# Optimization experiments

Hardware: AMD Instinct MI355X
Metric: run time of the kernel (lower is better)

The kernel has to match this reference:

```python
import jax, jax.numpy as jnp
import numpy as np

SIGNAL_SIZE = 33554432  # 2**25
N_ELEMENTS = 25         # log2(SIGNAL_SIZE)


def fft_shift(a, shift):
    # Faithful port of the torch fft_shift (note: 'shift' variable is reused
    # in the original; the phase ramp overwrites it after shift_samples).
    shift = 1.0 - shift
    n_samples = a.shape[-1]
    shift_samples = shift * n_samples * 0.5
    spec = jnp.fft.rfft(a, norm='ortho')
    n_coeffs = spec.shape[-1]
    phase = jnp.arange(n_coeffs) * (2j * np.pi / n_coeffs)  # complex64 ramp
    spec = spec * jnp.exp(phase * shift_samples)
    return jnp.fft.irfft(spec, n=n_samples, norm='ortho')


def setup_inputs() -> dict:
    key = jax.random.key(0)
    elements = jax.random.uniform(key, (N_ELEMENTS,), minval=-1.0, maxval=1.0,
                                  dtype=jnp.float32)
    return {"elements": elements}


def reference(elements):
    # dirac impulse of size 2 at position 0
    signal = jnp.zeros(2, dtype=jnp.float32).at[0].set(1.0)
    for i in range(N_ELEMENTS):  # fixed trip count; sizes double each step
        if i > 0:
            new_signal = jnp.zeros(signal.shape[-1] * 2, dtype=signal.dtype)
            signal = new_signal.at[::2].set(signal)
        shift_factor = 1.0 / (2 ** i)
        signal = fft_shift(signal, elements[i] * shift_factor)
    return signal  # shape [SIGNAL_SIZE]
```

## Files before the change

### kernel.cpp

```cpp
#include <hip/hip_runtime.h>


constexpr float PI_F    = 3.14159265358979323846f;
constexpr float TWOPI_F = 6.28318530717958647692f;
constexpr unsigned M24 = 1u << 24;

__device__ __forceinline__ void phase_sincos(float th, float* sn, float* cs) {
    double d = (double)th * 0.15915494309189533577;
    d -= rint(d);
    float ang = (float)(d * 6.2831853071795864769);
    __sincosf(ang, sn, cs);
}

__device__ __forceinline__ float2 cmul(float2 a, float2 f) {
    return make_float2(a.x * f.x - a.y * f.y, a.x * f.y + a.y * f.x);
}

__device__ __forceinline__ int xcd_swizzle(int b, int nblocks) {
    int chunk = nblocks >> 3;
    return (b & 7) * chunk + (b >> 3);
}

__global__ __launch_bounds__(256) void build_q(const float* __restrict__ el,
                                               float2* __restrict__ Q) {
    __shared__ float c_s[18], s_s[18], T_s[18];
    int tid = threadIdx.x;
    if (tid < 18) {
        float e = el[tid];
        float shift1 = e * (1.0f / (float)(1u << tid));
        float sh2 = 1.0f - shift1;
        float s = sh2 * (float)(1u << tid);
        float c = (float)(6.2831853071795864769 / (double)((1u << tid) + 1u));
        c_s[tid] = c;
        s_s[tid] = s;
        float p  = (float)(1u << tid) * c;
        float th = p * s;
        float sn, cs; phase_sincos(th, &sn, &cs);
        T_s[tid] = cs;
    }
    __syncthreads();

    unsigned r = blockIdx.x * 256u + (unsigned)tid;
    if (r == 0u) { Q[0] = make_float2(1.0f, 0.0f); return; }

    unsigned t = (unsigned)__builtin_ctz(r);
    float Pr = T_s[t], Pi = 0.0f;

#pragma unroll
    for (int i = 1; i <= 17; ++i) {
        unsigned hi = 1u << i;
        int sd = (int)((r + hi) & (2u * hi - 1u)) - (int)hi;
        int K  = (i <= (int)t) ? 0 : (sd < 0 ? -sd : sd);
        float sgn = (sd < 0) ? -1.0f : 1.0f;
        float p  = (float)K * c_s[i];
        float th = p * s_s[i];
        float sn, cs; phase_sincos(th, &sn, &cs);
        float ssn = sgn * sn;
        float nr = Pr * cs - Pi * ssn;
        float ni = Pr * ssn + Pi * cs;
        Pr = nr; Pi = ni;
    }
    Q[r] = make_float2(Pr, Pi);
}

__device__ __forceinline__ float2 chain_factor(int i, unsigned k,
                                               const float* __restrict__ c_s,
                                               const float* __restrict__ s_s) {
    unsigned hi = 1u << i;
    int sd = (int)((k + hi) & (2u * hi - 1u)) - (int)hi;
    int K  = (sd < 0) ? -sd : sd;
    float sgn = (sd < 0) ? -1.0f : 1.0f;
    float p  = (float)K * c_s[i];
    float th = p * s_s[i];
    float sn, cs; phase_sincos(th, &sn, &cs);
    return make_float2(cs, sgn * sn);
}

struct WPair { float2 wk, wmk; };

__device__ __forceinline__ WPair chain_tail(unsigned k, float Pr, float Pi,
                                            const float* __restrict__ c_s,
                                            const float* __restrict__ s_s) {
    const float sc = 1.0f / 33554432.0f;
    unsigned mk = M24 - k;
    float thk = ((float)k  * c_s[24]) * s_s[24];
    float thm = ((float)mk * c_s[24]) * s_s[24];
    float snk, csk, snm, csm;
    phase_sincos(thk, &snk, &csk);
    phase_sincos(thm, &snm, &csm);

    float Skr = Pr * csk - Pi * snk;
    float Ski = Pr * snk + Pi * csk;
    float Smr = Pr * csm + Pi * snm;
    float Smi = Pr * snm - Pi * csm;

    float Ar = Skr + Smr, Ai = Ski - Smi;
    float Br = Skr - Smr, Bi = Ski + Smi;
    float ang = (float)k * (TWOPI_F / 33554432.0f);
    float ts, tc; __sincosf(ang, &ts, &tc);
    float Cr = tc * Br - ts * Bi;
    float Ci = ts * Br + tc * Bi;

    WPair w;
    w.wk  = make_float2((Ar - Ci) * sc, (Ai + Cr) * sc);
    w.wmk = make_float2((Ar + Ci) * sc, (Cr - Ai) * sc);
    return w;
}

__device__ __forceinline__ WPair chain_W(unsigned k,
                                         const float* __restrict__ c_s,
                                         const float* __restrict__ s_s,
                                         const float* __restrict__ T_s,
                                         const float2* __restrict__ Q) {
    unsigned t = (unsigned)__builtin_ctz(k);
    unsigned r = k & 0x3FFFFu;
    float Pr, Pi;
    if (r != 0u) {
        float2 q = Q[r];
        Pr = q.x; Pi = q.y;
    } else {
        Pr = T_s[t]; Pi = 0.0f;
    }
#pragma unroll
    for (int i = 18; i <= 23; ++i) {
        unsigned hi = 1u << i;
        int sd = (int)((k + hi) & (2u * hi - 1u)) - (int)hi;
        int K  = (i <= (int)t) ? 0 : (sd < 0 ? -sd : sd);
        float sgn = (sd < 0) ? -1.0f : 1.0f;
        float p  = (float)K * c_s[i];
        float th = p * s_s[i];
        float sn, cs; phase_sincos(th, &sn, &cs);
        float ssn = sgn * sn;
        float nr = Pr * cs - Pi * ssn;
        float ni = Pr * ssn + Pi * cs;
        Pr = nr; Pi = ni;
    }
    return chain_tail(k, Pr, Pi, c_s, s_s);
}

__device__ __forceinline__ void bf4(float2* __restrict__ row, int e0, int d,
                                    float2 tw, float2 tw2) {
    float2 x0 = row[e0], x1 = row[e0 + d], x2 = row[e0 + 2*d], x3 = row[e0 + 3*d];
    float2 a0 = make_float2(x0.x + x2.x, x0.y + x2.y);
    float2 d0 = make_float2(x0.x - x2.x, x0.y - x2.y);
    float2 a1 = make_float2(x1.x + x3.x, x1.y + x3.y);
    float2 d1 = make_float2(x1.x - x3.x, x1.y - x3.y);
    float2 a2 = make_float2(d0.x * tw.x - d0.y * tw.y,  d0.x * tw.y + d0.y * tw.x);
    float2 a3 = make_float2(-d1.x * tw.y - d1.y * tw.x, d1.x * tw.x - d1.y * tw.y);
    row[e0]       = make_float2(a0.x + a1.x, a0.y + a1.y);
    float2 u1 = make_float2(a0.x - a1.x, a0.y - a1.y);
    row[e0 + d]   = make_float2(u1.x * tw2.x - u1.y * tw2.y, u1.x * tw2.y + u1.y * tw2.x);
    row[e0 + 2*d] = make_float2(a2.x + a3.x, a2.y + a3.y);
    float2 u3 = make_float2(a2.x - a3.x, a2.y - a3.y);
    row[e0 + 3*d] = make_float2(u3.x * tw2.x - u3.y * tw2.y, u3.x * tw2.y + u3.y * tw2.x);
}

__device__ __forceinline__ void fft256x16_inv(float2 (*lds)[257], int tid) {
    {
        int j2 = tid & 63;
        float s, c; __sincosf((PI_F / 128.0f) * (float)j2, &s, &c);
        float2 tw  = make_float2(c, s);
        float2 tw2 = make_float2(c * c - s * s, 2.0f * c * s);
        __syncthreads();
#pragma unroll
        for (int v = 0; v < 4; ++v) {
            int row = (tid >> 6) + 4 * v;
            bf4(lds[row], j2, 64, tw, tw2);
        }
    }
    {
        int rowb = tid & 15;
        int j2   = tid >> 4;
        float s, c; __sincosf((PI_F / 32.0f) * (float)j2, &s, &c);
        float2 tw  = make_float2(c, s);
        float2 tw2 = make_float2(c * c - s * s, 2.0f * c * s);
        __syncthreads();
#pragma unroll
        for (int v = 0; v < 4; ++v) {
            bf4(lds[rowb], 64 * v + j2, 16, tw, tw2);
        }
    }
    {
        int rowb = tid & 15;
        int j2   = tid >> 6;
        int bbl  = (tid >> 4) & 3;
        float s, c; __sincosf((PI_F / 8.0f) * (float)j2, &s, &c);
        float2 tw  = make_float2(c, s);
        float2 tw2 = make_float2(c * c - s * s, 2.0f * c * s);
        __syncthreads();
#pragma unroll
        for (int v = 0; v < 4; ++v) {
            int bb = bbl + 4 * v;
            bf4(lds[rowb], 16 * bb + j2, 4, tw, tw2);
        }
    }
    {
        int rowb = tid & 15;
        int bbl  = tid >> 4;
        __syncthreads();
#pragma unroll
        for (int v = 0; v < 4; ++v) {
            int e0 = 4 * (bbl + 16 * v);
            float2* row = lds[rowb];
            float2 x0 = row[e0], x1 = row[e0 + 1], x2 = row[e0 + 2], x3 = row[e0 + 3];
            float2 a0 = make_float2(x0.x + x2.x, x0.y + x2.y);
            float2 d0 = make_float2(x0.x - x2.x, x0.y - x2.y);
            float2 a1 = make_float2(x1.x + x3.x, x1.y + x3.y);
            float2 d1 = make_float2(x1.x - x3.x, x1.y - x3.y);
            row[e0]     = make_float2(a0.x + a1.x, a0.y + a1.y);
            row[e0 + 1] = make_float2(a0.x - a1.x, a0.y - a1.y);
            row[e0 + 2] = make_float2(d0.x - d1.y, d0.y + d1.x);
            row[e0 + 3] = make_float2(d0.x + d1.y, d0.y - d1.x);
        }
    }
    __syncthreads();
}

__device__ __forceinline__ int c_of_row(int b, int r) {
    if (b == 0) {
        if (r < 8)  return r;
        if (r == 8) return 32768;
        return 65536 - (r - 8);
    }
    return (r < 8) ? (8 * b + r) : (65536 - 8 * b - (r - 8));
}

__global__ __launch_bounds__(256, 4) void fused_build_fft_a(const float* __restrict__ el,
                                                            const float2* __restrict__ Q,
                                                            float2* __restrict__ out) {
    __shared__ float2 lds[16][257];
    __shared__ float c_s[25], s_s[25], T_s[24];
    int tid = threadIdx.x;
    if (tid < 25) {
        float e = el[tid];
        float shift1 = e * (1.0f / (float)(1u << tid));
        float sh2 = 1.0f - shift1;
        float s = sh2 * (float)(1u << tid);
        float c = (float)(6.2831853071795864769 / (double)((1u << tid) + 1u));
        c_s[tid] = c;
        s_s[tid] = s;
        if (tid < 24) {
            float p  = (float)(1u << tid) * c;
            float th = p * s;
            float sn, cs; phase_sincos(th, &sn, &cs);
            T_s[tid] = cs;
        }
    }
    __syncthreads();

    int b   = xcd_swizzle(blockIdx.x, 4096);
    int r   = tid & 15;
    int k30 = tid >> 4;
    int c   = c_of_row(b, r);
    int rm  = (b == 0 && (r == 0 || r == 8)) ? r : (r ^ 8);

    if (b == 0 && r == 0) {
#pragma unroll 1
        for (int u = 0; u < 8; ++u) {
            int k3 = k30 + 16 * u;
            if (k3 == 0) {
                float p  = 16777216.0f * c_s[24];
                float th = p * s_s[24];
                float sn, cs; phase_sincos(th, &sn, &cs);
                const float sc = 1.0f / 33554432.0f;
                lds[0][0] = make_float2((1.0f + cs) * sc, (1.0f - cs) * sc);
                WPair w = chain_W(8388608u, c_s, s_s, T_s, Q);
                lds[0][128] = w.wk;
            } else {
                unsigned j = (unsigned)k3 << 16;
                WPair w = chain_W(j, c_s, s_s, T_s, Q);
                lds[0][k3] = w.wk;
                lds[0][256 - k3] = w.wmk;
            }
        }
    } else {
        unsigned kbase = (unsigned)c + ((unsigned)k30 << 16);
        unsigned rres  = kbase & 0x3FFFFu;
        float2 P1 = Q[rres];
        P1 = cmul(P1, chain_factor(18, kbase, c_s, s_s));
        P1 = cmul(P1, chain_factor(19, kbase, c_s, s_s));
        float2 P2[2], P3[4];
#pragma unroll
        for (int j = 0; j < 2; ++j)
            P2[j] = cmul(P1, chain_factor(20, kbase + ((unsigned)j << 20), c_s, s_s));
#pragma unroll
        for (int j = 0; j < 4; ++j)
            P3[j] = cmul(P2[j & 1], chain_factor(21, kbase + ((unsigned)j << 20), c_s, s_s));

#pragma unroll 1
        for (int u = 0; u < 8; ++u) {
            int k3 = k30 + 16 * u;
            unsigned k = kbase + ((unsigned)u << 20);
            float2 P = cmul(P3[u & 3], chain_factor(22, k, c_s, s_s));
            P = cmul(P, chain_factor(23, k, c_s, s_s));
            WPair w = chain_tail(k, P.x, P.y, c_s, s_s);
            lds[r][k3] = w.wk;
            lds[rm][255 - k3] = w.wmk;
        }
    }

    fft256x16_inv(lds, tid);

#pragma unroll
    for (int u = 0; u < 16; ++u) {
        int e = tid + 256 * u;
        int row = e & 15, p = e >> 4;
        int t3 = (int)(__brev((unsigned)p) >> 24);
        int cr = c_of_row(b, row);
        out[cr + (t3 << 16)] = lds[row][p];
    }
}

__global__ __launch_bounds__(256, 4) void fft_stage_b(const float2* __restrict__ in,
                                                      float2* __restrict__ out) {
    __shared__ float2 lds[16][257];
    int tid = threadIdx.x;
    int wg  = xcd_swizzle(blockIdx.x, 4096);
    int k1b = (wg & 15) * 16;
    int t3  = wg >> 4;
    const float tsc = TWOPI_F / 65536.0f;
    {
        int row = tid & 15;
        int k20 = tid >> 4;
        const float2* src = in + (k1b + row + (k20 << 8) + (t3 << 16));
        float2 vbuf[16];
#pragma unroll
        for (int u = 0; u < 16; ++u) vbuf[u] = src[u << 12];
        float sb, cb; __sincosf(tsc * (float)(t3 * k20), &sb, &cb);
        float ss, cs; __sincosf(tsc * (float)(t3 * 16), &ss, &cs);
        float2 w = make_float2(cb, sb);
#pragma unroll
        for (int u = 0; u < 16; ++u) {
            int k2 = k20 + 16 * u;
            float2 v = vbuf[u];
            lds[row][k2] = make_float2(v.x * w.x - v.y * w.y, v.x * w.y + v.y * w.x);
            float nx = w.x * cs - w.y * ss;
            float ny = w.x * ss + w.y * cs;
            w = make_float2(nx, ny);
        }
    }
    fft256x16_inv(lds, tid);
#pragma unroll
    for (int u = 0; u < 16; ++u) {
        int e = tid + 256 * u;
        int row = e & 15, p = e >> 4;
        int t2 = (int)(__brev((unsigned)p) >> 24);
        out[k1b + row + (t2 << 8) + (t3 << 16)] = lds[row][p];
    }
}

__global__ __launch_bounds__(256, 4) void fft_stage_c(const float2* __restrict__ in,
                                                      float2* __restrict__ out) {
    __shared__ float2 lds[16][257];
    int tid = threadIdx.x;
    int wg  = xcd_swizzle(blockIdx.x, 4096);
    int t3b = (wg & 15) * 16;
    int t2  = wg >> 4;
    const float tsc = TWOPI_F / 16777216.0f;
    {
        int k1 = tid;
        const float2* src = in + (k1 + (t2 << 8) + (t3b << 16));
        float2 vbuf[16];
#pragma unroll
        for (int u = 0; u < 16; ++u) vbuf[u] = src[u << 16];
        int base = (t3b + (t2 << 8)) * k1;
        float sb, cb; __sincosf(tsc * (float)base, &sb, &cb);
        float ss, cs; __sincosf(tsc * (float)k1, &ss, &cs);
        float2 w = make_float2(cb, sb);
#pragma unroll
        for (int u = 0; u < 16; ++u) {
            float2 v = vbuf[u];
            lds[u][k1] = make_float2(v.x * w.x - v.y * w.y, v.x * w.y + v.y * w.x);
            float nx = w.x * cs - w.y * ss;
            float ny = w.x * ss + w.y * cs;
            w = make_float2(nx, ny);
        }
    }
    fft256x16_inv(lds, tid);
#pragma unroll
    for (int u = 0; u < 16; ++u) {
        int e = tid + 256 * u;
        int r = e & 15, p = e >> 4;
        int t1 = (int)(__brev((unsigned)p) >> 24);
        out[(t3b + r) + (t2 << 8) + (t1 << 16)] = lds[r][p];
    }
}

extern "C" void kernel_launch(void* const* d_in, const int* in_sizes, int n_in,
                              void* d_out, int out_size, void* d_ws, size_t ws_size,
                              hipStream_t stream) {
    const float* el = (const float*)d_in[0];
    float2* Gd = (float2*)d_out;
    float2* Q  = (float2*)d_ws;

    hipLaunchKernelGGL(build_q,           dim3(1024), dim3(256), 0, stream, el, Q);
    hipLaunchKernelGGL(fused_build_fft_a, dim3(4096), dim3(256), 0, stream, el, Q, Gd);
    hipLaunchKernelGGL(fft_stage_b,       dim3(4096), dim3(256), 0, stream, Gd, (float2*)d_ws);
    hipLaunchKernelGGL(fft_stage_c,       dim3(4096), dim3(256), 0, stream, (float2*)d_ws, Gd);
}
```

Baseline: 278.4 us.

## Replace radix-4 LDS FFT passes with register-resident radix-16 two-pass FFT

Replaces the four-pass radix-4 256-point FFT, which round-trips through shared memory each pass, with a 16x16 decomposition. Each thread holds 16 values in registers, applies a radix-16 butterfly, twiddles, transposes once through LDS, then does a second radix-16 pass. The final bit-reversed LDS readback is dropped and results are written straight to global memory. Stage B also keeps its loaded data in registers for the first pass. Launch bounds drop from 4 to 3 blocks per CU to make room for the larger register footprint. This cuts LDS traffic and barriers at the cost of higher register pressure and less regular store coalescing.

```diff
diff --git a/kernel.cpp b/kernel.cpp
--- a/kernel.cpp
+++ b/kernel.cpp
@@ -1,7 +1,6 @@
 #include <hip/hip_runtime.h>
 
 
-constexpr float PI_F    = 3.14159265358979323846f;
 constexpr float TWOPI_F = 6.28318530717958647692f;
 constexpr unsigned M24 = 1u << 24;
 
@@ -15,10 +14,65 @@
 __device__ __forceinline__ float2 cmul(float2 a, float2 f) {
     return make_float2(a.x * f.x - a.y * f.y, a.x * f.y + a.y * f.x);
 }
+__device__ __forceinline__ float2 caddf(float2 a, float2 b) { return make_float2(a.x + b.x, a.y + b.y); }
+__device__ __forceinline__ float2 csubf(float2 a, float2 b) { return make_float2(a.x - b.x, a.y - b.y); }
+__device__ __forceinline__ float2 cmulw(float2 a, float c, float s) {
+    return make_float2(a.x * c - a.y * s, a.x * s + a.y * c);
+}
 
 __device__ __forceinline__ int xcd_swizzle(int b, int nblocks) {
     int chunk = nblocks >> 3;
     return (b & 7) * chunk + (b >> 3);
+}
+
+__device__ __forceinline__ void fft16_inv(float2* v) {
+    const float C1 = 0.92387953251128675613f;
+    const float S1 = 0.38268343236508977173f;
+    const float R2 = 0.70710678118654752440f;
+    float2 h[16];
+#pragma unroll
+    for (int b = 0; b < 4; ++b) {
+        float2 s02 = caddf(v[b], v[b + 8]);
+        float2 d02 = csubf(v[b], v[b + 8]);
+        float2 s13 = caddf(v[b + 4], v[b + 12]);
+        float2 d13 = csubf(v[b + 4], v[b + 12]);
+        float2 id13 = make_float2(-d13.y, d13.x);
+        h[4 * b + 0] = caddf(s02, s13);
+        h[4 * b + 1] = caddf(d02, id13);
+        h[4 * b + 2] = csubf(s02, s13);
+        h[4 * b + 3] = csubf(d02, id13);
+    }
+    h[5]  = cmulw(h[5],  C1,  S1);
+    h[6]  = make_float2(R2 * (h[6].x - h[6].y),  R2 * (h[6].x + h[6].y));
+    h[7]  = cmulw(h[7],  S1,  C1);
+    h[9]  = make_float2(R2 * (h[9].x - h[9].y),  R2 * (h[9].x + h[9].y));
+    h[10] = make_float2(-h[10].y, h[10].x);
+    h[11] = cmulw(h[11], -R2, R2);
+    h[13] = cmulw(h[13], S1,  C1);
+    h[14] = cmulw(h[14], -R2, R2);
+    h[15] = cmulw(h[15], -C1, -S1);
+#pragma unroll
+    for (int K1 = 0; K1 < 4; ++K1) {
+        float2 a = h[K1], bb = h[4 + K1], cc = h[8 + K1], dd = h[12 + K1];
+        float2 sac = caddf(a, cc), dac = csubf(a, cc);
+        float2 sbd = caddf(bb, dd), dbd = csubf(bb, dd);
+        float2 idbd = make_float2(-dbd.y, dbd.x);
+        v[K1]      = caddf(sac, sbd);
+        v[K1 + 4]  = caddf(dac, idbd);
+        v[K1 + 8]  = csubf(sac, sbd);
+        v[K1 + 12] = csubf(dac, idbd);
+    }
+}
+
+__device__ __forceinline__ void ztwiddle(float2* v, int q) {
+    float ss, cc;
+    __sincosf((TWOPI_F / 256.0f) * (float)q, &ss, &cc);
+    float2 w = make_float2(1.0f, 0.0f), stp = make_float2(cc, ss);
+#pragma unroll
+    for (int K1 = 0; K1 < 16; ++K1) {
+        v[K1] = cmul(v[K1], w);
+        w = cmul(w, stp);
+    }
 }
 
 __global__ __launch_bounds__(256) void build_q(const float* __restrict__ el,
@@ -138,84 +192,6 @@
     return chain_tail(k, Pr, Pi, c_s, s_s);
 }
 
-__device__ __forceinline__ void bf4(float2* __restrict__ row, int e0, int d,
-                                    float2 tw, float2 tw2) {
-    float2 x0 = row[e0], x1 = row[e0 + d], x2 = row[e0 + 2*d], x3 = row[e0 + 3*d];
-    float2 a0 = make_float2(x0.x + x2.x, x0.y + x2.y);
-    float2 d0 = make_float2(x0.x - x2.x, x0.y - x2.y);
-    float2 a1 = make_float2(x1.x + x3.x, x1.y + x3.y);
-    float2 d1 = make_float2(x1.x - x3.x, x1.y - x3.y);
-    float2 a2 = make_float2(d0.x * tw.x - d0.y * tw.y,  d0.x * tw.y + d0.y * tw.x);
-    float2 a3 = make_float2(-d1.x * tw.y - d1.y * tw.x, d1.x * tw.x - d1.y * tw.y);
-    row[e0]       = make_float2(a0.x + a1.x, a0.y + a1.y);
-    float2 u1 = make_float2(a0.x - a1.x, a0.y - a1.y);
-    row[e0 + d]   = make_float2(u1.x * tw2.x - u1.y * tw2.y, u1.x * tw2.y + u1.y * tw2.x);
-    row[e0 + 2*d] = make_float2(a2.x + a3.x, a2.y + a3.y);
-    float2 u3 = make_float2(a2.x - a3.x, a2.y - a3.y);
-    row[e0 + 3*d] = make_float2(u3.x * tw2.x - u3.y * tw2.y, u3.x * tw2.y + u3.y * tw2.x);
-}
-
-__device__ __forceinline__ void fft256x16_inv(float2 (*lds)[257], int tid) {
-    {
-        int j2 = tid & 63;
-        float s, c; __sincosf((PI_F / 128.0f) * (float)j2, &s, &c);
-        float2 tw  = make_float2(c, s);
-        float2 tw2 = make_float2(c * c - s * s, 2.0f * c * s);
-        __syncthreads();
-#pragma unroll
-        for (int v = 0; v < 4; ++v) {
-            int row = (tid >> 6) + 4 * v;
-            bf4(lds[row], j2, 64, tw, tw2);
-        }
-    }
-    {
-        int rowb = tid & 15;
-        int j2   = tid >> 4;
-        float s, c; __sincosf((PI_F / 32.0f) * (float)j2, &s, &c);
-        float2 tw  = make_float2(c, s);
-        float2 tw2 = make_float2(c * c - s * s, 2.0f * c * s);
-        __syncthreads();
-#pragma unroll
-        for (int v = 0; v < 4; ++v) {
-            bf4(lds[rowb], 64 * v + j2, 16, tw, tw2);
-        }
-    }
-    {
-        int rowb = tid & 15;
-        int j2   = tid >> 6;
-        int bbl  = (tid >> 4) & 3;
-        float s, c; __sincosf((PI_F / 8.0f) * (float)j2, &s, &c);
-        float2 tw  = make_float2(c, s);
-        float2 tw2 = make_float2(c * c - s * s, 2.0f * c * s);
-        __syncthreads();
-#pragma unroll
-        for (int v = 0; v < 4; ++v) {
-            int bb = bbl + 4 * v;
-            bf4(lds[rowb], 16 * bb + j2, 4, tw, tw2);
-        }
-    }
-    {
-        int rowb = tid & 15;
-        int bbl  = tid >> 4;
-        __syncthreads();
-#pragma unroll
-        for (int v = 0; v < 4; ++v) {
-            int e0 = 4 * (bbl + 16 * v);
-            float2* row = lds[rowb];
-            float2 x0 = row[e0], x1 = row[e0 + 1], x2 = row[e0 + 2], x3 = row[e0 + 3];
-            float2 a0 = make_float2(x0.x + x2.x, x0.y + x2.y);
-            float2 d0 = make_float2(x0.x - x2.x, x0.y - x2.y);
-            float2 a1 = make_float2(x1.x + x3.x, x1.y + x3.y);
-            float2 d1 = make_float2(x1.x - x3.x, x1.y - x3.y);
-            row[e0]     = make_float2(a0.x + a1.x, a0.y + a1.y);
-            row[e0 + 1] = make_float2(a0.x - a1.x, a0.y - a1.y);
-            row[e0 + 2] = make_float2(d0.x - d1.y, d0.y + d1.x);
-            row[e0 + 3] = make_float2(d0.x + d1.y, d0.y - d1.x);
-        }
-    }
-    __syncthreads();
-}
-
 __device__ __forceinline__ int c_of_row(int b, int r) {
     if (b == 0) {
         if (r < 8)  return r;
@@ -225,7 +201,7 @@
     return (r < 8) ? (8 * b + r) : (65536 - 8 * b - (r - 8));
 }
 
-__global__ __launch_bounds__(256, 4) void fused_build_fft_a(const float* __restrict__ el,
+__global__ __launch_bounds__(256, 3) void fused_build_fft_a(const float* __restrict__ el,
                                                             const float2* __restrict__ Q,
                                                             float2* __restrict__ out) {
     __shared__ float2 lds[16][257];
@@ -248,16 +224,16 @@
     }
     __syncthreads();
 
-    int b   = xcd_swizzle(blockIdx.x, 4096);
-    int r   = tid & 15;
-    int k30 = tid >> 4;
-    int c   = c_of_row(b, r);
-    int rm  = (b == 0 && (r == 0 || r == 8)) ? r : (r ^ 8);
+    int b = xcd_swizzle(blockIdx.x, 4096);
+    int r = tid & 15;
+    int q = tid >> 4;
+    int c = c_of_row(b, r);
+    int rm = (b == 0 && (r == 0 || r == 8)) ? r : (r ^ 8);
 
     if (b == 0 && r == 0) {
 #pragma unroll 1
         for (int u = 0; u < 8; ++u) {
-            int k3 = k30 + 16 * u;
+            int k3 = q + 16 * u;
             if (k3 == 0) {
                 float p  = 16777216.0f * c_s[24];
                 float th = p * s_s[24];
@@ -274,7 +250,7 @@
             }
         }
     } else {
-        unsigned kbase = (unsigned)c + ((unsigned)k30 << 16);
+        unsigned kbase = (unsigned)c + ((unsigned)q << 16);
         unsigned rres  = kbase & 0x3FFFFu;
         float2 P1 = Q[rres];
         P1 = cmul(P1, chain_factor(18, kbase, c_s, s_s));
@@ -289,7 +265,7 @@
 
 #pragma unroll 1
         for (int u = 0; u < 8; ++u) {
-            int k3 = k30 + 16 * u;
+            int k3 = q + 16 * u;
             unsigned k = kbase + ((unsigned)u << 20);
             float2 P = cmul(P3[u & 3], chain_factor(22, k, c_s, s_s));
             P = cmul(P, chain_factor(23, k, c_s, s_s));
@@ -298,20 +274,26 @@
             lds[rm][255 - k3] = w.wmk;
         }
     }
-
-    fft256x16_inv(lds, tid);
-
-#pragma unroll
-    for (int u = 0; u < 16; ++u) {
-        int e = tid + 256 * u;
-        int row = e & 15, p = e >> 4;
-        int t3 = (int)(__brev((unsigned)p) >> 24);
-        int cr = c_of_row(b, row);
-        out[cr + (t3 << 16)] = lds[row][p];
-    }
-}
-
-__global__ __launch_bounds__(256, 4) void fft_stage_b(const float2* __restrict__ in,
+    __syncthreads();
+
+    float2 v[16];
+#pragma unroll
+    for (int n1 = 0; n1 < 16; ++n1) v[n1] = lds[r][q + 16 * n1];
+    fft16_inv(v);
+    ztwiddle(v, q);
+#pragma unroll
+    for (int K1 = 0; K1 < 16; ++K1) lds[r][K1 * 16 + q] = v[K1];
+    __syncthreads();
+
+#pragma unroll
+    for (int n2 = 0; n2 < 16; ++n2) v[n2] = lds[r][q * 16 + n2];
+    fft16_inv(v);
+#pragma unroll
+    for (int K2 = 0; K2 < 16; ++K2)
+        out[c + ((q + 16 * K2) << 16)] = v[K2];
+}
+
+__global__ __launch_bounds__(256, 3) void fft_stage_b(const float2* __restrict__ in,
                                                       float2* __restrict__ out) {
     __shared__ float2 lds[16][257];
     int tid = threadIdx.x;
@@ -319,37 +301,39 @@
     int k1b = (wg & 15) * 16;
     int t3  = wg >> 4;
     const float tsc = TWOPI_F / 65536.0f;
+    int row = tid & 15;
+    int q   = tid >> 4;
+
+    float2 v[16];
+    const float2* src = in + (k1b + row + (q << 8) + (t3 << 16));
+#pragma unroll
+    for (int u = 0; u < 16; ++u) v[u] = src[u << 12];
+
     {
-        int row = tid & 15;
-        int k20 = tid >> 4;
-        const float2* src = in + (k1b + row + (k20 << 8) + (t3 << 16));
-        float2 vbuf[16];
-#pragma unroll
-        for (int u = 0; u < 16; ++u) vbuf[u] = src[u << 12];
-        float sb, cb; __sincosf(tsc * (float)(t3 * k20), &sb, &cb);
-        float ss, cs; __sincosf(tsc * (float)(t3 * 16), &ss, &cs);
-        float2 w = make_float2(cb, sb);
+        float sb, cb; __sincosf(tsc * (float)(t3 * q), &sb, &cb);
+        float ssx, csx; __sincosf(tsc * (float)(t3 * 16), &ssx, &csx);
+        float2 w = make_float2(cb, sb), stp = make_float2(csx, ssx);
 #pragma unroll
         for (int u = 0; u < 16; ++u) {
-            int k2 = k20 + 16 * u;
-            float2 v = vbuf[u];
-            lds[row][k2] = make_float2(v.x * w.x - v.y * w.y, v.x * w.y + v.y * w.x);
-            float nx = w.x * cs - w.y * ss;
-            float ny = w.x * ss + w.y * cs;
-            w = make_float2(nx, ny);
-        }
-    }
-    fft256x16_inv(lds, tid);
-#pragma unroll
-    for (int u = 0; u < 16; ++u) {
-        int e = tid + 256 * u;
-        int row = e & 15, p = e >> 4;
-        int t2 = (int)(__brev((unsigned)p) >> 24);
-        out[k1b + row + (t2 << 8) + (t3 << 16)] = lds[row][p];
-    }
-}
-
-__global__ __launch_bounds__(256, 4) void fft_stage_c(const float2* __restrict__ in,
+            v[u] = cmul(v[u], w);
+            w = cmul(w, stp);
+        }
+    }
+    fft16_inv(v);
+    ztwiddle(v, q);
+#pragma unroll
+    for (int K1 = 0; K1 < 16; ++K1) lds[row][K1 * 16 + q] = v[K1];
+    __syncthreads();
+
+#pragma unroll
+    for (int n2 = 0; n2 < 16; ++n2) v[n2] = lds[row][q * 16 + n2];
+    fft16_inv(v);
+#pragma unroll
+    for (int K2 = 0; K2 < 16; ++K2)
+        out[k1b + row + ((q + 16 * K2) << 8) + (t3 << 16)] = v[K2];
+}
+
+__global__ __launch_bounds__(256, 3) void fft_stage_c(const float2* __restrict__ in,
                                                       float2* __restrict__ out) {
     __shared__ float2 lds[16][257];
     int tid = threadIdx.x;
@@ -357,33 +341,42 @@
     int t3b = (wg & 15) * 16;
     int t2  = wg >> 4;
     const float tsc = TWOPI_F / 16777216.0f;
+
     {
         int k1 = tid;
         const float2* src = in + (k1 + (t2 << 8) + (t3b << 16));
-        float2 vbuf[16];
-#pragma unroll
-        for (int u = 0; u < 16; ++u) vbuf[u] = src[u << 16];
+        float2 vb[16];
+#pragma unroll
+        for (int u = 0; u < 16; ++u) vb[u] = src[u << 16];
         int base = (t3b + (t2 << 8)) * k1;
         float sb, cb; __sincosf(tsc * (float)base, &sb, &cb);
-        float ss, cs; __sincosf(tsc * (float)k1, &ss, &cs);
-        float2 w = make_float2(cb, sb);
+        float ssx, csx; __sincosf(tsc * (float)k1, &ssx, &csx);
+        float2 w = make_float2(cb, sb), stp = make_float2(csx, ssx);
 #pragma unroll
         for (int u = 0; u < 16; ++u) {
-            float2 v = vbuf[u];
-            lds[u][k1] = make_float2(v.x * w.x - v.y * w.y, v.x * w.y + v.y * w.x);
-            float nx = w.x * cs - w.y * ss;
-            float ny = w.x * ss + w.y * cs;
-            w = make_float2(nx, ny);
-        }
-    }
-    fft256x16_inv(lds, tid);
-#pragma unroll
-    for (int u = 0; u < 16; ++u) {
-        int e = tid + 256 * u;
-        int r = e & 15, p = e >> 4;
-        int t1 = (int)(__brev((unsigned)p) >> 24);
-        out[(t3b + r) + (t2 << 8) + (t1 << 16)] = lds[r][p];
-    }
+            lds[u][k1] = cmul(vb[u], w);
+            w = cmul(w, stp);
+        }
+    }
+    __syncthreads();
+
+    int rr = tid & 15;
+    int q  = tid >> 4;
+    float2 v[16];
+#pragma unroll
+    for (int n1 = 0; n1 < 16; ++n1) v[n1] = lds[rr][q + 16 * n1];
+    fft16_inv(v);
+    ztwiddle(v, q);
+#pragma unroll
+    for (int K1 = 0; K1 < 16; ++K1) lds[rr][K1 * 16 + q] = v[K1];
+    __syncthreads();
+
+#pragma unroll
+    for (int n2 = 0; n2 < 16; ++n2) v[n2] = lds[rr][q * 16 + n2];
+    fft16_inv(v);
+#pragma unroll
+    for (int K2 = 0; K2 < 16; ++K2)
+        out[(t3b + rr) + (t2 << 8) + ((q + 16 * K2) << 16)] = v[K2];
 }
 
 extern "C" void kernel_launch(void* const* d_in, const int* in_sizes, int n_in,
```

New measurement: 270.9 us. -2.7%, faster.
